# Optimization experiments

Measured on AMD Instinct MI355X. Metric: run time of the kernel, lower is better.

The kernel has to match this reference:

```python
import jax, jax.numpy as jnp
import numpy as np

N_HEAD = 16
EPS = 1e-5

def _layernorm(x, g, b):
    m = jnp.mean(x, axis=-1, keepdims=True)
    v = jnp.mean((x - m) ** 2, axis=-1, keepdims=True)
    return (x - m) * jax.lax.rsqrt(v + EPS) * g + b

def _gru_gate(h, X, w, u, bz):
    # w, u: [3, C, C] stacked (r, z, h) matrices; matches torch.tensordot(X, W, dims=1)
    r = jax.nn.sigmoid(X @ w[0] + h @ u[0])
    z = jax.nn.sigmoid(X @ w[1] + h @ u[1] - bz)
    h_next = jnp.tanh(X @ w[2] + (h * r) @ u[2])
    return (1.0 - z) * h + z * h_next

def setup_inputs() -> dict:
    key = jax.random.key(0)
    B, T, C = 4, 1024, 1024
    ks = jax.random.split(key, 32)
    s = 0.02
    inp = {
        'q': jax.random.normal(ks[0], (B, T, C), jnp.float32),
        'k': jax.random.normal(ks[1], (B, T, C), jnp.float32),
        'v': jax.random.normal(ks[2], (B, T, C), jnp.float32),
        'ln1_g': jnp.ones((C,), jnp.float32), 'ln1_b': jnp.zeros((C,), jnp.float32),
        'ln2_g': jnp.ones((C,), jnp.float32), 'ln2_b': jnp.zeros((C,), jnp.float32),
        'Wq': jax.random.normal(ks[3], (C, C), jnp.float32) * s, 'bq': jnp.zeros((C,), jnp.float32),
        'Wk': jax.random.normal(ks[4], (C, C), jnp.float32) * s, 'bk': jnp.zeros((C,), jnp.float32),
        'Wv': jax.random.normal(ks[5], (C, C), jnp.float32) * s, 'bv': jnp.zeros((C,), jnp.float32),
        'Wp': jax.random.normal(ks[6], (C, C), jnp.float32) * s, 'bp': jnp.zeros((C,), jnp.float32),
        'W1': jax.random.normal(ks[7], (C, 2 * C), jnp.float32) * s, 'b1': jnp.zeros((2 * C,), jnp.float32),
        'W2': jax.random.normal(ks[8], (2 * C, C), jnp.float32) * s, 'b2': jnp.zeros((C,), jnp.float32),
        'g1_w': jax.random.normal(ks[9], (3, C, C), jnp.float32) * s,
        'g1_u': jax.random.normal(ks[10], (3, C, C), jnp.float32) * s,
        'g1_bz': jnp.full((C,), 2.0, jnp.float32),  # init_gru_gate_bias
        'g2_w': jax.random.normal(ks[11], (3, C, C), jnp.float32) * s,
        'g2_u': jax.random.normal(ks[12], (3, C, C), jnp.float32) * s,
        'g2_bz': jnp.full((C,), 2.0, jnp.float32),
    }
    return inp

def reference(q, k, v, ln1_g, ln1_b, ln2_g, ln2_b, Wq, bq, Wk, bk, Wv, bv, Wp, bp,
              W1, b1, W2, b2, g1_w, g1_u, g1_bz, g2_w, g2_u, g2_bz):
    B, T, C = q.shape
    D = C // N_HEAD
    qn = _layernorm(q, ln1_g, ln1_b)
    kn = _layernorm(k, ln1_g, ln1_b)
    vn = _layernorm(v, ln1_g, ln1_b)
    qh = (qn @ Wq + bq).reshape(B, T, N_HEAD, D)
    kh = (kn @ Wk + bk).reshape(B, T, N_HEAD, D)
    vh = (vn @ Wv + bv).reshape(B, T, N_HEAD, D)
    att = jnp.einsum('bqhd,bkhd->bhqk', qh, kh) * (1.0 / np.sqrt(D))
    causal = jnp.tril(jnp.ones((T, T), bool))  # mask[-Tq:, :Tk]
    att_scores = jnp.where(causal, att, -jnp.inf)
    att_probs = jax.nn.softmax(att_scores, axis=-1)
    y = jnp.einsum('bhqk,bkhd->bqhd', att_probs, vh).reshape(B, T, C)
    att_out = y @ Wp + bp
    x = _gru_gate(q, att_out, g1_w, g1_u, g1_bz)
    h = _layernorm(x, ln2_g, ln2_b)
    mlp = jax.nn.gelu(h @ W1 + b1, approximate=False) @ W2 + b2
    x = _gru_gate(x, mlp, g2_w, g2_u, g2_bz)
    return (x, att_scores)
```

## Files before the change

kernel.cpp:

```cpp
#include <hip/hip_runtime.h>
#include <math.h>

#define TDIM 1024
#define CDIM 1024
#define NHEAD 16
#define HD 64
#define MROWS 4096

#define MASK_NEG -1.0e30f

typedef __attribute__((ext_vector_type(8))) __bf16 bf16x8;
typedef __attribute__((ext_vector_type(4))) float f32x4;

__device__ __forceinline__ float sigf(float x) { return 1.0f / (1.0f + expf(-x)); }
__device__ __forceinline__ float geluf(float x) { return x * 0.5f * (1.0f + erff(x * 0.7071067811865475f)); }
__device__ __forceinline__ float bf2f(unsigned short u) {
    union { unsigned u; float f; } x; x.u = ((unsigned)u) << 16; return x.f;
}
__device__ __forceinline__ unsigned short f2bf(float f) {
    union { float f; unsigned u; } x; x.f = f;
    unsigned r = x.u + 0x7FFFu + ((x.u >> 16) & 1u);
    return (unsigned short)(r >> 16);
}

__global__ __launch_bounds__(256) void wconv_t(const float* __restrict__ i0,
                                               const float* __restrict__ i1,
                                               const float* __restrict__ i2,
                                               const float* __restrict__ i3,
                                               int gper,
                                               unsigned short* __restrict__ out,
                                               int K, int N) {
    int z = blockIdx.z;
    int sel = z / gper, sub = z % gper;
    const float* ps = sel == 0 ? i0 : sel == 1 ? i1 : sel == 2 ? i2 : i3;
    const float* inb = ps + (size_t)sub * K * N;
    unsigned short* outb = out + (size_t)z * K * N;
    __shared__ float tile[32][33];
    int t = threadIdx.x;
    int r = t >> 3, c = (t & 7) * 4;
    int kb = blockIdx.y * 32, nb = blockIdx.x * 32;
    float4 vv = *(const float4*)(inb + (size_t)(kb + r) * N + nb + c);
    tile[r][c + 0] = vv.x; tile[r][c + 1] = vv.y; tile[r][c + 2] = vv.z; tile[r][c + 3] = vv.w;
    __syncthreads();
    ushort4 o;
    o.x = f2bf(tile[c + 0][r]); o.y = f2bf(tile[c + 1][r]);
    o.z = f2bf(tile[c + 2][r]); o.w = f2bf(tile[c + 3][r]);
    *(ushort4*)(outb + (size_t)(nb + r) * K + kb + c) = o;
}

__global__ __launch_bounds__(256) void ln3_kernel(const float* __restrict__ p0,
                                                  const float* __restrict__ p1,
                                                  const float* __restrict__ p2,
                                                  const float* __restrict__ g,
                                                  const float* __restrict__ b,
                                                  unsigned short* __restrict__ out,
                                                  unsigned short* __restrict__ qb) {
    int row = blockIdx.x, z = blockIdx.y;
    const float* xr = (z == 0 ? p0 : z == 1 ? p1 : p2) + (size_t)row * CDIM;
    int t = threadIdx.x;
    float4 v = *(const float4*)(xr + t * 4);
    if (z == 0) {
        ushort4 o; o.x = f2bf(v.x); o.y = f2bf(v.y); o.z = f2bf(v.z); o.w = f2bf(v.w);
        *(ushort4*)(qb + (size_t)row * CDIM + t * 4) = o;
    }
    __shared__ float red[256];
    red[t] = v.x + v.y + v.z + v.w;
    __syncthreads();
    for (int o = 128; o > 0; o >>= 1) { if (t < o) red[t] += red[t + o]; __syncthreads(); }
    float mean = red[0] * (1.0f / CDIM);
    __syncthreads();
    float dx = v.x - mean, dy = v.y - mean, dz = v.z - mean, dw = v.w - mean;
    red[t] = dx * dx + dy * dy + dz * dz + dw * dw;
    __syncthreads();
    for (int o = 128; o > 0; o >>= 1) { if (t < o) red[t] += red[t + o]; __syncthreads(); }
    float var = red[0] * (1.0f / CDIM);
    float inv = 1.0f / sqrtf(var + 1e-5f);
    float4 gv = *(const float4*)(g + t * 4);
    float4 bv = *(const float4*)(b + t * 4);
    ushort4 o4;
    o4.x = f2bf(dx * inv * gv.x + bv.x);
    o4.y = f2bf(dy * inv * gv.y + bv.y);
    o4.z = f2bf(dz * inv * gv.z + bv.z);
    o4.w = f2bf(dw * inv * gv.w + bv.w);
    *(ushort4*)(out + ((size_t)z * MROWS + row) * CDIM + t * 4) = o4;
}

struct GemmZ {
    const unsigned short* A;
    const unsigned short* Bt;
    const float* bias;
    unsigned short* C;
    int ldC;
    int om;
    int gelu;
    int pad;
};
struct GemmDesc { GemmZ z0, z1, z2, z3, z4; };

__global__ __launch_bounds__(256) void mfma_gemmz(GemmDesc d, int M, int N, int K) {
    __shared__ unsigned short As[2][128 * 32];
    __shared__ unsigned short Bs[2][128 * 32];
    GemmZ zz;
    switch (blockIdx.z) {
        case 0: zz = d.z0; break;
        case 1: zz = d.z1; break;
        case 2: zz = d.z2; break;
        case 3: zz = d.z3; break;
        default: zz = d.z4; break;
    }
    const unsigned short* A = zz.A;
    const unsigned short* Bt = zz.Bt;

    int t = threadIdx.x;
    int wave = t >> 6, lane = t & 63;
    int nwg = gridDim.x * gridDim.y;
    int hID = blockIdx.y * gridDim.x + blockIdx.x;
    int nl = (hID & 7) * (nwg >> 3) + (hID >> 3);
    int bx = nl % gridDim.x, by = nl / gridDim.x;
    int m0 = by * 128, n0 = bx * 128;
    int wx = wave & 1, wy = wave >> 1;
    int srow = lane >> 2;
    int scol = (lane & 3) * 8;
    int fr = lane & 15;
    int fq = (lane >> 4) * 8;

    f32x4 acc[4][4] = {};

#define STAGE_AB(buf, k0v)                                                                         \
    {                                                                                              \
        _Pragma("unroll")                                                                          \
        for (int i = 0; i < 2; i++) {                                                              \
            int rt = (wave * 2 + i) * 16 + srow;                                                   \
            __builtin_amdgcn_global_load_lds(                                                      \
                (const __attribute__((address_space(1))) void*)(A + (size_t)(m0 + rt) * K + (k0v) + scol), \
                (__attribute__((address_space(3))) void*)(As[buf] + rt * 32 + scol), 16, 0, 0);    \
            __builtin_amdgcn_global_load_lds(                                                      \
                (const __attribute__((address_space(1))) void*)(Bt + (size_t)(n0 + rt) * K + (k0v) + scol), \
                (__attribute__((address_space(3))) void*)(Bs[buf] + rt * 32 + scol), 16, 0, 0);    \
        }                                                                                          \
    }

    STAGE_AB(0, 0);
    int cur = 0;
    for (int k0 = 0; k0 < K; k0 += 32) {
        __syncthreads();
        if (k0 + 32 < K) STAGE_AB(cur ^ 1, k0 + 32);

        bf16x8 af[4], bfr[4];
#pragma unroll
        for (int mi = 0; mi < 4; mi++)
            af[mi] = *(const bf16x8*)(As[cur] + (wy * 64 + mi * 16 + fr) * 32 + fq);
#pragma unroll
        for (int ni = 0; ni < 4; ni++)
            bfr[ni] = *(const bf16x8*)(Bs[cur] + (wx * 64 + ni * 16 + fr) * 32 + fq);
#pragma unroll
        for (int mi = 0; mi < 4; mi++)
#pragma unroll
            for (int ni = 0; ni < 4; ni++)
                acc[mi][ni] = __builtin_amdgcn_mfma_f32_16x16x32_bf16(af[mi], bfr[ni], acc[mi][ni], 0, 0, 0);
        cur ^= 1;
    }
#undef STAGE_AB

    int col_l = lane & 15, quad = lane >> 4;
#pragma unroll
    for (int ni = 0; ni < 4; ni++) {
        int c = n0 + wx * 64 + ni * 16 + col_l;
        float bb = zz.bias ? zz.bias[c] : 0.0f;
#pragma unroll
        for (int mi = 0; mi < 4; mi++) {
#pragma unroll
            for (int r = 0; r < 4; r++) {
                int row = m0 + wy * 64 + mi * 16 + quad * 4 + r;
                float vv = acc[mi][ni][r] + bb;
                if (zz.gelu) vv = geluf(vv);
                size_t idx;
                if (zz.om == 1) {
                    int bI = row >> 10, tt2 = row & 1023, hh = c >> 6, dd = c & 63;
                    idx = (((size_t)(bI * NHEAD + hh)) * TDIM + tt2) * HD + dd;
                } else if (zz.om == 2) {
                    int bI = row >> 10, tt2 = row & 1023, hh = c >> 6, dd = c & 63;
                    idx = (((size_t)(bI * NHEAD + hh)) * HD + dd) * TDIM + tt2;
                } else {
                    idx = (size_t)row * zz.ldC + c;
                }
                zz.C[idx] = f2bf(vv);
            }
        }
    }
}

__global__ __launch_bounds__(256, 4) void attn_fused(const unsigned short* __restrict__ Q,
                                                     const unsigned short* __restrict__ K,
                                                     const unsigned short* __restrict__ Vt,
                                                     float* __restrict__ S,
                                                     unsigned short* __restrict__ Y) {
    int hID = blockIdx.y * gridDim.x + blockIdx.x;
    int nlw = (hID & 7) * 128 + (hID >> 3);
    int qt = nlw & 15, bh = nlw >> 4;
    int q0 = qt * 64;
    int t = threadIdx.x, w = t >> 6, lane = t & 63;
    int l15 = lane & 15, quad = lane >> 4;
    int l7 = lane & 7, l3 = lane >> 3;

    __shared__ unsigned short Ks[2][4096];
    __shared__ unsigned short Vs[2][4096];
    __shared__ unsigned short PsU[4096];

    const unsigned short* Qb = Q + ((size_t)bh * TDIM + q0) * HD;
    const unsigned short* Kb0 = K + (size_t)bh * TDIM * HD;
    const unsigned short* Vtb = Vt + (size_t)bh * HD * TDIM;
    float* Sb = S + (size_t)bh * TDIM * TDIM;

    int dstoff = w * 512 + lane * 8;

    bf16x8 aq[2];
    {
        int qrow = w * 16 + l15;
#pragma unroll
        for (int kk = 0; kk < 2; kk++)
            aq[kk] = *(const bf16x8*)(Qb + (size_t)qrow * HD + kk * 32 + quad * 8);
    }

    float m_run[4], l_run[4];
    f32x4 yacc[4];
#pragma unroll
    for (int r = 0; r < 4; r++) { m_run[r] = MASK_NEG; l_run[r] = 0.f; }
#pragma unroll
    for (int nd = 0; nd < 4; nd++) yacc[nd] = (f32x4){0.f, 0.f, 0.f, 0.f};

    unsigned short* Psw = PsU + w * 1024;

#define STAGE_KV(buf, ktile)                                                                        \
    {                                                                                               \
        _Pragma("unroll")                                                                           \
        for (int it = 0; it < 2; it++) {                                                            \
            int row = it * 32 + w * 8 + l3;                                        \
            __builtin_amdgcn_global_load_lds(                                                       \
                (const __attribute__((address_space(1))) void*)(Kb0 + (size_t)((ktile) * 64 + row) * HD + ((l7 ^ l3) << 3)), \
                (__attribute__((address_space(3))) void*)(Ks[buf] + it * 2048 + dstoff), 16, 0, 0); \
            __builtin_amdgcn_global_load_lds(                                                       \
                (const __attribute__((address_space(1))) void*)(Vtb + (size_t)row * TDIM + (ktile) * 64 + ((l7 ^ l3) << 3)), \
                (__attribute__((address_space(3))) void*)(Vs[buf] + it * 2048 + dstoff), 16, 0, 0); \
        }                                                                                           \
    }

    STAGE_KV(0, 0);
    int cur = 0;

    for (int kt = 0; kt <= qt; kt++) {
        __syncthreads();
        if (kt < qt) STAGE_KV(cur ^ 1, kt + 1);

        f32x4 sA[4];
#pragma unroll
        for (int n = 0; n < 4; n++) sA[n] = (f32x4){0.f, 0.f, 0.f, 0.f};
        __builtin_amdgcn_s_setprio(1);
#pragma unroll
        for (int kk = 0; kk < 2; kk++) {
#pragma unroll
            for (int n = 0; n < 4; n++) {
                int krow = n * 16 + l15;
                bf16x8 bk = *(const bf16x8*)(Ks[cur] + krow * 64 + ((((kk * 64 + quad * 16)) ^ ((krow & 7) << 4)) >> 1));
                sA[n] = __builtin_amdgcn_mfma_f32_16x16x32_bf16(aq[kk], bk, sA[n], 0, 0, 0);
            }
        }
        __builtin_amdgcn_s_setprio(0);

        int kbase = kt * 64;
        bool diag = (kt == qt);
#pragma unroll
        for (int n = 0; n < 4; n++) {
            int kg = kbase + n * 16 + l15;
#pragma unroll
            for (int r = 0; r < 4; r++) {
                int qg = q0 + w * 16 + quad * 4 + r;
                float x = sA[n][r] * 0.125f;
                if (diag && kg > qg) x = MASK_NEG;
                sA[n][r] = x;
                Sb[(size_t)qg * TDIM + kg] = x;
            }
        }

#pragma unroll
        for (int r = 0; r < 4; r++) {
            float m = fmaxf(fmaxf(sA[0][r], sA[1][r]), fmaxf(sA[2][r], sA[3][r]));
            m = fmaxf(m, __shfl_xor(m, 1));
            m = fmaxf(m, __shfl_xor(m, 2));
            m = fmaxf(m, __shfl_xor(m, 4));
            m = fmaxf(m, __shfl_xor(m, 8));
            float mn = fmaxf(m_run[r], m);
            float sc = expf(m_run[r] - mn);
            m_run[r] = mn;
            float ls = 0.f;
#pragma unroll
            for (int n = 0; n < 4; n++) {
                float p = expf(sA[n][r] - mn);
                sA[n][r] = p;
                ls += p;
            }
            ls += __shfl_xor(ls, 1);
            ls += __shfl_xor(ls, 2);
            ls += __shfl_xor(ls, 4);
            ls += __shfl_xor(ls, 8);
            l_run[r] = l_run[r] * sc + ls;
#pragma unroll
            for (int nd = 0; nd < 4; nd++) yacc[nd][r] *= sc;
        }

#pragma unroll
        for (int n = 0; n < 4; n++) {
            int kk2 = n * 16 + l15;
#pragma unroll
            for (int r = 0; r < 4; r++) {
                int qq = quad * 4 + r;
                Psw[qq * 64 + (((kk2 * 2) ^ ((qq & 7) << 4)) >> 1)] = f2bf(sA[n][r]);
            }
        }

        __builtin_amdgcn_s_setprio(1);
#pragma unroll
        for (int kk = 0; kk < 2; kk++) {
            bf16x8 pa = *(const bf16x8*)(Psw + l15 * 64 + ((((kk * 64 + quad * 16)) ^ ((l15 & 7) << 4)) >> 1));
#pragma unroll
            for (int nd = 0; nd < 4; nd++) {
                int dr = nd * 16 + l15;
                bf16x8 bv = *(const bf16x8*)(Vs[cur] + dr * 64 + ((((kk * 64 + quad * 16)) ^ ((dr & 7) << 4)) >> 1));
                yacc[nd] = __builtin_amdgcn_mfma_f32_16x16x32_bf16(pa, bv, yacc[nd], 0, 0, 0);
            }
        }
        __builtin_amdgcn_s_setprio(0);
        cur ^= 1;
    }
#undef STAGE_KV

    int bI = bh >> 4, h = bh & 15;
#pragma unroll
    for (int r = 0; r < 4; r++) {
        float inv = 1.0f / l_run[r];
        int row = bI * TDIM + q0 + w * 16 + quad * 4 + r;
#pragma unroll
        for (int nd = 0; nd < 4; nd++)
            Y[(size_t)row * CDIM + h * HD + nd * 16 + l15] = f2bf(yacc[nd][r] * inv);
    }

    int kfill = (qt + 1) * 64;
    if (kfill < TDIM) {
        float4 m4 = make_float4(MASK_NEG, MASK_NEG, MASK_NEG, MASK_NEG);
        int rr = t >> 4, cc = (t & 15) * 4;
#pragma unroll
        for (int rp = 0; rp < 4; rp++) {
            float* Srow = Sb + (size_t)(q0 + rp * 16 + rr) * TDIM;
            for (int k4 = kfill + cc; k4 < TDIM; k4 += 64)
                *(float4*)(Srow + k4) = m4;
        }
    }
}

__global__ __launch_bounds__(256) void ew_r(const unsigned short* __restrict__ A1, int ldA,
                                            const unsigned short* __restrict__ B1,
                                            const unsigned short* __restrict__ h,
                                            unsigned short* __restrict__ out) {
    int row = blockIdx.x, c = threadIdx.x * 4;
    ushort4 a = *(const ushort4*)(A1 + (size_t)row * ldA + c);
    size_t i = (size_t)row * CDIM + c;
    ushort4 b = *(const ushort4*)(B1 + i);
    ushort4 hh = *(const ushort4*)(h + i);
    ushort4 o;
    o.x = f2bf(bf2f(hh.x) * sigf(bf2f(a.x) + bf2f(b.x)));
    o.y = f2bf(bf2f(hh.y) * sigf(bf2f(a.y) + bf2f(b.y)));
    o.z = f2bf(bf2f(hh.z) * sigf(bf2f(a.z) + bf2f(b.z)));
    o.w = f2bf(bf2f(hh.w) * sigf(bf2f(a.w) + bf2f(b.w)));
    *(ushort4*)(out + i) = o;
}

template <int F32OUT, int DOLN>
__global__ __launch_bounds__(256) void ew_final2(const unsigned short* __restrict__ A, int ldA,
                                                 const unsigned short* __restrict__ B2p,
                                                 const unsigned short* __restrict__ B3v,
                                                 const unsigned short* __restrict__ h,
                                                 const float* __restrict__ bz,
                                                 void* __restrict__ out,
                                                 const float* __restrict__ lng,
                                                 const float* __restrict__ lnb,
                                                 unsigned short* __restrict__ lnout) {
    int row = blockIdx.x, t = threadIdx.x, c = t * 4;
    size_t ia = (size_t)row * ldA;
    size_t i = (size_t)row * CDIM + c;
    ushort4 a2 = *(const ushort4*)(A + ia + 1024 + c);
    ushort4 b2 = *(const ushort4*)(B2p + i);
    ushort4 a3 = *(const ushort4*)(A + ia + 2048 + c);
    ushort4 b3 = *(const ushort4*)(B3v + i);
    ushort4 hh = *(const ushort4*)(h + i);
    float4 bzv = *(const float4*)(bz + c);
    float zz, o0, o1, o2, o3;
    zz = sigf(bf2f(a2.x) + bf2f(b2.x) - bzv.x); o0 = (1.f - zz) * bf2f(hh.x) + zz * tanhf(bf2f(a3.x) + bf2f(b3.x));
    zz = sigf(bf2f(a2.y) + bf2f(b2.y) - bzv.y); o1 = (1.f - zz) * bf2f(hh.y) + zz * tanhf(bf2f(a3.y) + bf2f(b3.y));
    zz = sigf(bf2f(a2.z) + bf2f(b2.z) - bzv.z); o2 = (1.f - zz) * bf2f(hh.z) + zz * tanhf(bf2f(a3.z) + bf2f(b3.z));
    zz = sigf(bf2f(a2.w) + bf2f(b2.w) - bzv.w); o3 = (1.f - zz) * bf2f(hh.w) + zz * tanhf(bf2f(a3.w) + bf2f(b3.w));
    if (F32OUT) {
        *(float4*)((float*)out + i) = make_float4(o0, o1, o2, o3);
    } else {
        ushort4 o; o.x = f2bf(o0); o.y = f2bf(o1); o.z = f2bf(o2); o.w = f2bf(o3);
        *(ushort4*)((unsigned short*)out + i) = o;
    }
    if (DOLN) {
        __shared__ float red[256];
        red[t] = o0 + o1 + o2 + o3;
        __syncthreads();
        for (int o = 128; o > 0; o >>= 1) { if (t < o) red[t] += red[t + o]; __syncthreads(); }
        float mean = red[0] * (1.0f / CDIM);
        __syncthreads();
        float dx = o0 - mean, dy = o1 - mean, dz = o2 - mean, dw = o3 - mean;
        red[t] = dx * dx + dy * dy + dz * dz + dw * dw;
        __syncthreads();
        for (int o = 128; o > 0; o >>= 1) { if (t < o) red[t] += red[t + o]; __syncthreads(); }
        float var = red[0] * (1.0f / CDIM);
        float inv = 1.0f / sqrtf(var + 1e-5f);
        float4 gv = *(const float4*)(lng + c);
        float4 bv = *(const float4*)(lnb + c);
        ushort4 o4;
        o4.x = f2bf(dx * inv * gv.x + bv.x);
        o4.y = f2bf(dy * inv * gv.y + bv.y);
        o4.z = f2bf(dz * inv * gv.z + bv.z);
        o4.w = f2bf(dw * inv * gv.w + bv.w);
        *(ushort4*)(lnout + i) = o4;
    }
}

extern "C" void kernel_launch(void* const* d_in, const int* in_sizes, int n_in,
                              void* d_out, int out_size, void* d_ws, size_t ws_size,
                              hipStream_t stream) {
    const float* q    = (const float*)d_in[0];
    const float* k    = (const float*)d_in[1];
    const float* v    = (const float*)d_in[2];
    const float* ln1g = (const float*)d_in[3];
    const float* ln1b = (const float*)d_in[4];
    const float* ln2g = (const float*)d_in[5];
    const float* ln2b = (const float*)d_in[6];
    const float* Wq   = (const float*)d_in[7];
    const float* bq   = (const float*)d_in[8];
    const float* Wk   = (const float*)d_in[9];
    const float* bk   = (const float*)d_in[10];
    const float* Wv   = (const float*)d_in[11];
    const float* bv   = (const float*)d_in[12];
    const float* Wp   = (const float*)d_in[13];
    const float* bp   = (const float*)d_in[14];
    const float* W1   = (const float*)d_in[15];
    const float* b1   = (const float*)d_in[16];
    const float* W2   = (const float*)d_in[17];
    const float* b2   = (const float*)d_in[18];
    const float* g1w  = (const float*)d_in[19];
    const float* g1u  = (const float*)d_in[20];
    const float* g1bz = (const float*)d_in[21];
    const float* g2w  = (const float*)d_in[22];
    const float* g2u  = (const float*)d_in[23];
    const float* g2bz = (const float*)d_in[24];

    float* out_x = (float*)d_out;
    float* out_s = out_x + (size_t)MROWS * CDIM;

    unsigned short* w = (unsigned short*)d_ws;
    const size_t MM = (size_t)CDIM * CDIM;
    unsigned short* wWq  = w;
    unsigned short* wWk  = w + 1 * MM;
    unsigned short* wWv  = w + 2 * MM;
    unsigned short* wWp  = w + 3 * MM;
    unsigned short* wW1  = w + 4 * MM;
    unsigned short* wW2  = w + 6 * MM;
    unsigned short* wg1w = w + 8 * MM;
    unsigned short* wg1u = w + 11 * MM;
    unsigned short* wg2w = w + 14 * MM;
    unsigned short* wg2u = w + 17 * MM;
    unsigned short* act = w + 20 * MM;
    const size_t SLOT = (size_t)MROWS * CDIM;
    unsigned short* s0 = act + 0 * SLOT;
    unsigned short* s1 = act + 1 * SLOT;
    unsigned short* s2 = act + 2 * SLOT;
    unsigned short* s3 = act + 3 * SLOT;
    unsigned short* s4 = act + 4 * SLOT;
    unsigned short* s5 = act + 5 * SLOT;
    unsigned short* s6 = act + 6 * SLOT;
    unsigned short* s7 = act + 7 * SLOT;
    unsigned short* s8 = act + 8 * SLOT;
    (void)s4; (void)wWk; (void)wWv;

    dim3 blk(256);
    dim3 g_attn(16, 64);
    dim3 g_ew(MROWS);

    auto mkz = [](const unsigned short* A, const unsigned short* Bt, const float* bias,
                  unsigned short* C, int ldC, int om, int gelu) {
        GemmZ z; z.A = A; z.Bt = Bt; z.bias = bias; z.C = C; z.ldC = ldC; z.om = om;
        z.gelu = gelu; z.pad = 0; return z;
    };

    wconv_t<<<dim3(32, 32, 4), blk, 0, stream>>>(Wq, Wk, Wv, Wp, 1, wWq, 1024, 1024);
    wconv_t<<<dim3(32, 32, 12), blk, 0, stream>>>(g1w, g1u, g2w, g2u, 3, wg1w, 1024, 1024);
    wconv_t<<<dim3(64, 32, 1), blk, 0, stream>>>(W1, W1, W1, W1, 1, wW1, 1024, 2048);
    wconv_t<<<dim3(32, 64, 1), blk, 0, stream>>>(W2, W2, W2, W2, 1, wW2, 2048, 1024);

    ln3_kernel<<<dim3(MROWS, 3), blk, 0, stream>>>(q, k, v, ln1g, ln1b, s0, s6);

    {
        GemmDesc dd = { mkz(s0, wWq, bq, s3, 0, 1, 0),
                        mkz(s1, wWq + 1 * MM, bk, s4, 0, 1, 0),
                        mkz(s2, wWq + 2 * MM, bv, s5, 0, 2, 0),
                        mkz(s6, wg1u + 0 * MM, nullptr, s7, CDIM, 0, 0),
                        mkz(s6, wg1u + 1 * MM, nullptr, s8, CDIM, 0, 0) };
        mfma_gemmz<<<dim3(8, 32, 5), blk, 0, stream>>>(dd, MROWS, CDIM, CDIM);
    }

    attn_fused<<<g_attn, blk, 0, stream>>>(s3, s4, s5, out_s, s0);

    {
        GemmDesc dd = { mkz(s0, wWp, bp, s1, CDIM, 0, 0),
                        mkz(s0, wWp, bp, s1, CDIM, 0, 0), mkz(s0, wWp, bp, s1, CDIM, 0, 0),
                        mkz(s0, wWp, bp, s1, CDIM, 0, 0), mkz(s0, wWp, bp, s1, CDIM, 0, 0) };
        mfma_gemmz<<<dim3(8, 32, 1), blk, 0, stream>>>(dd, MROWS, CDIM, CDIM);
    }

    {
        GemmDesc dd = { mkz(s1, wg1w + 0 * MM, nullptr, s2, 3 * CDIM, 0, 0),
                        mkz(s1, wg1w + 1 * MM, nullptr, s2 + CDIM, 3 * CDIM, 0, 0),
                        mkz(s1, wg1w + 2 * MM, nullptr, s2 + 2 * CDIM, 3 * CDIM, 0, 0),
                        mkz(s1, wg1w, nullptr, s2, 3 * CDIM, 0, 0),
                        mkz(s1, wg1w, nullptr, s2, 3 * CDIM, 0, 0) };
        mfma_gemmz<<<dim3(8, 32, 3), blk, 0, stream>>>(dd, MROWS, CDIM, CDIM);
    }
    ew_r<<<g_ew, blk, 0, stream>>>(s2, 3 * CDIM, s7, s6, s5);
    {
        GemmDesc dd = { mkz(s5, wg1u + 2 * MM, nullptr, s0, CDIM, 0, 0),
                        mkz(s5, wg1u + 2 * MM, nullptr, s0, CDIM, 0, 0),
                        mkz(s5, wg1u + 2 * MM, nullptr, s0, CDIM, 0, 0),
                        mkz(s5, wg1u + 2 * MM, nullptr, s0, CDIM, 0, 0),
                        mkz(s5, wg1u + 2 * MM, nullptr, s0, CDIM, 0, 0) };
        mfma_gemmz<<<dim3(8, 32, 1), blk, 0, stream>>>(dd, MROWS, CDIM, CDIM);
    }
    ew_final2<0, 1><<<g_ew, blk, 0, stream>>>(s2, 3 * CDIM, s8, s0, s6, g1bz,
                                              s1, ln2g, ln2b, s5);

    {
        GemmDesc dd = { mkz(s5, wW1, b1, s3, 2 * CDIM, 0, 1),
                        mkz(s5, wW1 + MM, b1 + 1024, s3 + CDIM, 2 * CDIM, 0, 1),
                        mkz(s1, wg2u + 0 * MM, nullptr, s6, CDIM, 0, 0),
                        mkz(s1, wg2u + 1 * MM, nullptr, s7, CDIM, 0, 0),
                        mkz(s5, wW1, b1, s3, 2 * CDIM, 0, 1) };
        mfma_gemmz<<<dim3(8, 32, 4), blk, 0, stream>>>(dd, MROWS, CDIM, CDIM);
    }
    {
        GemmDesc dd = { mkz(s3, wW2, b2, s0, CDIM, 0, 0),
                        mkz(s3, wW2, b2, s0, CDIM, 0, 0), mkz(s3, wW2, b2, s0, CDIM, 0, 0),
                        mkz(s3, wW2, b2, s0, CDIM, 0, 0), mkz(s3, wW2, b2, s0, CDIM, 0, 0) };
        mfma_gemmz<<<dim3(8, 32, 1), blk, 0, stream>>>(dd, MROWS, CDIM, 2 * CDIM);
    }
    {
        GemmDesc dd = { mkz(s0, wg2w + 0 * MM, nullptr, s2, 3 * CDIM, 0, 0),
                        mkz(s0, wg2w + 1 * MM, nullptr, s2 + CDIM, 3 * CDIM, 0, 0),
                        mkz(s0, wg2w + 2 * MM, nullptr, s2 + 2 * CDIM, 3 * CDIM, 0, 0),
                        mkz(s0, wg2w, nullptr, s2, 3 * CDIM, 0, 0),
                        mkz(s0, wg2w, nullptr, s2, 3 * CDIM, 0, 0) };
        mfma_gemmz<<<dim3(8, 32, 3), blk, 0, stream>>>(dd, MROWS, CDIM, CDIM);
    }
    ew_r<<<g_ew, blk, 0, stream>>>(s2, 3 * CDIM, s6, s1, s5);
    {
        GemmDesc dd = { mkz(s5, wg2u + 2 * MM, nullptr, s8, CDIM, 0, 0),
                        mkz(s5, wg2u + 2 * MM, nullptr, s8, CDIM, 0, 0),
                        mkz(s5, wg2u + 2 * MM, nullptr, s8, CDIM, 0, 0),
                        mkz(s5, wg2u + 2 * MM, nullptr, s8, CDIM, 0, 0),
                        mkz(s5, wg2u + 2 * MM, nullptr, s8, CDIM, 0, 0) };
        mfma_gemmz<<<dim3(8, 32, 1), blk, 0, stream>>>(dd, MROWS, CDIM, CDIM);
    }
    ew_final2<1, 0><<<g_ew, blk, 0, stream>>>(s2, 3 * CDIM, s7, s8, s1, g2bz,
                                              out_x, nullptr, nullptr, nullptr);
}
```

Baseline: 909.5 us.

## Triple-buffer GEMM LDS staging with partial vmcnt waits

Moves the bf16 MFMA GEMM from double to triple buffering in shared memory, prefetching two K-tiles ahead. Each iteration waits only until the oldest tile has landed (vmcnt(4)) instead of draining all loads, so global-to-LDS copies overlap more with MFMA work. This raises LDS use per block from 32KB to 48KB, which may lower occupancy. The hand-counted vmcnt value has to match the number of outstanding load instructions issued per stage.

```diff
diff --git a/kernel.cpp b/kernel.cpp
--- a/kernel.cpp
+++ b/kernel.cpp
@@ -98,8 +98,8 @@
 struct GemmDesc { GemmZ z0, z1, z2, z3, z4; };
 
 __global__ __launch_bounds__(256) void mfma_gemmz(GemmDesc d, int M, int N, int K) {
-    __shared__ unsigned short As[2][128 * 32];
-    __shared__ unsigned short Bs[2][128 * 32];
+    __shared__ unsigned short As[3][128 * 32];
+    __shared__ unsigned short Bs[3][128 * 32];
     GemmZ zz;
     switch (blockIdx.z) {
         case 0: zz = d.z0; break;
@@ -140,27 +140,43 @@
         }                                                                                          \
     }
 
+#define GEMM_BODY(BI)                                                                              \
+    {                                                                                              \
+        bf16x8 af[4], bfr[4];                                                                      \
+        _Pragma("unroll")                                                                          \
+        for (int mi = 0; mi < 4; mi++)                                                             \
+            af[mi] = *(const bf16x8*)(As[BI] + (wy * 64 + mi * 16 + fr) * 32 + fq);                \
+        _Pragma("unroll")                                                                          \
+        for (int ni = 0; ni < 4; ni++)                                                             \
+            bfr[ni] = *(const bf16x8*)(Bs[BI] + (wx * 64 + ni * 16 + fr) * 32 + fq);               \
+        _Pragma("unroll")                                                                          \
+        for (int mi = 0; mi < 4; mi++)                                                             \
+            _Pragma("unroll")                                                                      \
+            for (int ni = 0; ni < 4; ni++)                                                         \
+                acc[mi][ni] = __builtin_amdgcn_mfma_f32_16x16x32_bf16(af[mi], bfr[ni], acc[mi][ni], 0, 0, 0); \
+    }
+
+    int nk = K >> 5;
     STAGE_AB(0, 0);
-    int cur = 0;
-    for (int k0 = 0; k0 < K; k0 += 32) {
-        __syncthreads();
-        if (k0 + 32 < K) STAGE_AB(cur ^ 1, k0 + 32);
-
-        bf16x8 af[4], bfr[4];
-#pragma unroll
-        for (int mi = 0; mi < 4; mi++)
-            af[mi] = *(const bf16x8*)(As[cur] + (wy * 64 + mi * 16 + fr) * 32 + fq);
-#pragma unroll
-        for (int ni = 0; ni < 4; ni++)
-            bfr[ni] = *(const bf16x8*)(Bs[cur] + (wx * 64 + ni * 16 + fr) * 32 + fq);
-#pragma unroll
-        for (int mi = 0; mi < 4; mi++)
-#pragma unroll
-            for (int ni = 0; ni < 4; ni++)
-                acc[mi][ni] = __builtin_amdgcn_mfma_f32_16x16x32_bf16(af[mi], bfr[ni], acc[mi][ni], 0, 0, 0);
-        cur ^= 1;
-    }
+    STAGE_AB(1, 32);
+    int bi = 0;
+    for (int k = 0; k < nk - 1; ++k) {
+        asm volatile("s_waitcnt vmcnt(4)" ::: "memory");
+        __builtin_amdgcn_s_barrier();
+        __builtin_amdgcn_sched_barrier(0);
+        if (k + 2 < nk) {
+            int tgt = bi + 2; if (tgt >= 3) tgt -= 3;
+            STAGE_AB(tgt, (k + 2) * 32);
+        }
+        GEMM_BODY(bi);
+        bi = bi + 1; if (bi == 3) bi = 0;
+    }
+    asm volatile("s_waitcnt vmcnt(0)" ::: "memory");
+    __builtin_amdgcn_s_barrier();
+    __builtin_amdgcn_sched_barrier(0);
+    GEMM_BODY(bi);
 #undef STAGE_AB
+#undef GEMM_BODY
 
     int col_l = lane & 15, quad = lane >> 4;
 #pragma unroll
```

After: 904.9 us. About the same (-0.5%).
